# Optimization experiments

Hardware: AMD Instinct MI355X
Metric: run time of the kernel (lower is better)

The kernel has to match this reference:

```python
import jax, jax.numpy as jnp
import numpy as np

EPS = 1e-5
LOSS_WEIGHT = 0.3
IGNORE_INDEX = -100


def rmsnorm(x, w):
    # x: (B,S,D), w: (D,)
    var = jnp.mean(x * x, axis=-1, keepdims=True)
    return x * jax.lax.rsqrt(var + EPS) * w


def cross_entropy(logits, targets):
    # logits: (B,T,V), targets: (B,T) int; ignore_index=-100, mean reduction
    logp = jax.nn.log_softmax(logits, axis=-1)
    valid = targets != IGNORE_INDEX
    safe_t = jnp.where(valid, targets, 0)
    nll = -jnp.take_along_axis(logp, safe_t[..., None], axis=-1)[..., 0]
    nll = jnp.where(valid, nll, 0.0)
    return jnp.sum(nll) / jnp.maximum(jnp.sum(valid), 1)


def setup_inputs() -> dict:
    key = jax.random.key(0)
    ks = jax.random.split(key, 5)
    B, S, D, V, H = 1, 2048, 1024, 50257, 3
    hidden = jax.random.normal(ks[0], (B, S, D), dtype=jnp.float32)
    targets = jax.random.randint(ks[1], (B, S), 0, V, dtype=jnp.int64)
    emb_w = jax.random.normal(ks[2], (V, D), dtype=jnp.float32) * 0.02
    main_norm_w = jnp.ones((D,), dtype=jnp.float32)
    aux_proj_w = jax.random.normal(ks[3], (H - 1, D, D), dtype=jnp.float32) * 0.02
    aux_norm_w = jnp.ones((H - 1, D), dtype=jnp.float32)
    aux_out_w = jax.random.normal(ks[4], (H - 1, V, D), dtype=jnp.float32) * 0.02
    return {"hidden": hidden, "targets": targets, "emb_w": emb_w,
            "main_norm_w": main_norm_w, "aux_proj_w": aux_proj_w,
            "aux_norm_w": aux_norm_w, "aux_out_w": aux_out_w}


def reference(hidden, targets, emb_w, main_norm_w, aux_proj_w, aux_norm_w, aux_out_w):
    # Main head: norm -> tied vocab projection
    main_logits = jnp.einsum('bsd,vd->bsv', rmsnorm(hidden, main_norm_w), emb_w)
    main_loss = cross_entropy(main_logits[:, :-1, :], targets[:, 1:])

    # Auxiliary heads predict t+2, t+3, ...
    n_aux = aux_proj_w.shape[0]
    aux_losses = []
    for i in range(n_aux):
        k = i + 2
        h = jnp.einsum('bsd,ed->bse', hidden, aux_proj_w[i])  # d_model -> d_model
        logits = jnp.einsum('bsd,vd->bsv', rmsnorm(h, aux_norm_w[i]), aux_out_w[i])
        aux_losses.append(cross_entropy(logits[:, :-k, :], targets[:, k:]))
    total_aux = sum(aux_losses) / len(aux_losses) if aux_losses else jnp.float32(0.0)
    loss = main_loss + LOSS_WEIGHT * total_aux
    return main_logits, loss
```

## Files before the change

kernel.cpp:

```cpp
#include <hip/hip_runtime.h>
#include <hip/hip_bf16.h>


typedef __hip_bfloat16 bf16;
typedef __attribute__((ext_vector_type(8))) short bf16x8;
typedef __attribute__((ext_vector_type(4))) float f32x4;

typedef const __attribute__((address_space(1))) void* gptr_t;
typedef __attribute__((address_space(3))) void* lptr_t;

#define S_LEN   2048
#define DMODEL  1024
#define VOCAB   50257
#define VPAD2   50432
#define NT256   197

__device__ __forceinline__ void gload_lds16(const void* g, void* l) {
  __builtin_amdgcn_global_load_lds((gptr_t)g, (lptr_t)l, 16, 0, 0);
}

__global__ __launch_bounds__(256) void k_cvt(const float* __restrict__ src,
                                             bf16* __restrict__ dst,
                                             long rows_src, long rows_pad) {
  const long total4 = rows_pad << 8;
  for (long i = (long)blockIdx.x * 256 + threadIdx.x; i < total4;
       i += (long)gridDim.x * 256) {
    const long e = i << 2;
    const long row = e >> 10;
    alignas(8) bf16 o[4];
    if (row < rows_src) {
      const float4 v = *(const float4*)(src + e);
      o[0] = __float2bfloat16(v.x); o[1] = __float2bfloat16(v.y);
      o[2] = __float2bfloat16(v.z); o[3] = __float2bfloat16(v.w);
    } else {
      o[0] = o[1] = o[2] = o[3] = __float2bfloat16(0.f);
    }
    *(uint2*)(dst + e) = *(const uint2*)o;
  }
}

__global__ __launch_bounds__(256) void k_rms(const float* __restrict__ x,
                                             const float* __restrict__ w,
                                             bf16* __restrict__ xn) {
  const int row = blockIdx.x;
  const int t = threadIdx.x;
  const float4 v = ((const float4*)(x + (size_t)row * DMODEL))[t];
  float ss = v.x*v.x + v.y*v.y + v.z*v.z + v.w*v.w;
  #pragma unroll
  for (int d = 1; d < 64; d <<= 1) ss += __shfl_xor(ss, d, 64);
  __shared__ float red[4];
  if ((t & 63) == 0) red[t >> 6] = ss;
  __syncthreads();
  const float tot = red[0] + red[1] + red[2] + red[3];
  const float scale = rsqrtf(tot * (1.f / DMODEL) + 1e-5f);
  const float4 wv = ((const float4*)w)[t];
  alignas(8) bf16 o[4];
  o[0] = __float2bfloat16(v.x * scale * wv.x);
  o[1] = __float2bfloat16(v.y * scale * wv.y);
  o[2] = __float2bfloat16(v.z * scale * wv.z);
  o[3] = __float2bfloat16(v.w * scale * wv.w);
  *(uint2*)(xn + (size_t)row * DMODEL + t * 4) = *(const uint2*)o;
}

template<bool WRITE_OUT, bool DO_CE>
__global__ __launch_bounds__(512, 2)
void k_gemm256(const bf16* __restrict__ A, const bf16* __restrict__ B,
               float* __restrict__ C, long ldc, int Nvalid,
               const int* __restrict__ targets, int shift,
               float* __restrict__ pmax, float* __restrict__ psum,
               float* __restrict__ ptgt, int ntiles) {
  __shared__ char lds[131072 + 9216];

  const int t = threadIdx.x;
  const int w = t >> 6, l = t & 63;
  const int g = l >> 4, q = l & 15;
  const int wr = w >> 2, wc = w & 3;
  const int bm = blockIdx.x, bn = blockIdx.y;

  f32x4 acc[8][4];
  #pragma unroll
  for (int i = 0; i < 8; ++i)
    #pragma unroll
    for (int j = 0; j < 4; ++j)
      #pragma unroll
      for (int r = 0; r < 4; ++r) acc[i][j][r] = 0.f;

  const int srow = (l >> 2);
  const int scol = ((l & 3) * 8) ^ (((l >> 5) & 1) * 16);
  const bf16* gA0 = A + (size_t)(bm * 256 + (w * 2 + 0) * 16 + srow) * DMODEL + scol;
  const bf16* gA1 = A + (size_t)(bm * 256 + (w * 2 + 1) * 16 + srow) * DMODEL + scol;
  const bf16* gB0 = B + (size_t)(bn * 256 + (w * 2 + 0) * 16 + srow) * DMODEL + scol;
  const bf16* gB1 = B + (size_t)(bn * 256 + (w * 2 + 1) * 16 + srow) * DMODEL + scol;

  auto stage = [&](int buf, int h, int tt) {
    const int kbase = tt * 64 + (h >> 1) * 32;
    char* lb = lds + buf * 65536 + (h >> 1) * 32768 + (h & 1) * 16384 + (w * 2) * 1024;
    if (h & 1) {
      gload_lds16(gB0 + kbase, lb);
      gload_lds16(gB1 + kbase, lb + 1024);
    } else {
      gload_lds16(gA0 + kbase, lb);
      gload_lds16(gA1 + kbase, lb + 1024);
    }
  };

  const int laneoff = (q * 64 + g * 16) ^ (((q >> 3) & 1) << 5);
  auto lda = [&](int buf, int kk, int mi) {
    return *(const bf16x8*)(lds + buf * 65536 + kk * 32768 + (wr * 8 + mi) * 1024 + laneoff);
  };
  auto ldb = [&](int buf, int kk, int ni) {
    return *(const bf16x8*)(lds + buf * 65536 + kk * 32768 + 16384 + (wc * 4 + ni) * 1024 + laneoff);
  };

  stage(0, 0, 0); stage(0, 1, 0); stage(0, 2, 0); stage(0, 3, 0);
  asm volatile("s_waitcnt vmcnt(4)" ::: "memory");
  __builtin_amdgcn_s_barrier();

  #define PHASE_MFMA(MH)                                                         \
    __builtin_amdgcn_s_barrier();                                                \
    __builtin_amdgcn_s_setprio(1);                                               \
    _Pragma("unroll")                                                            \
    for (int mi = 0; mi < 4; ++mi)                                               \
      _Pragma("unroll")                                                          \
      for (int ni = 0; ni < 4; ++ni)                                             \
        acc[(MH)*4 + mi][ni] = __builtin_amdgcn_mfma_f32_16x16x32_bf16(          \
            a[mi], b[ni], acc[(MH)*4 + mi][ni], 0, 0, 0);                        \
    __builtin_amdgcn_s_setprio(0);

  for (int tt = 0; tt < 16; ++tt) {
    const int buf = tt & 1, nbuf = buf ^ 1;
    const bool pre = tt < 15;
    bf16x8 a[4], b[4];

    #pragma unroll
    for (int mi = 0; mi < 4; ++mi) a[mi] = lda(buf, 0, mi);
    #pragma unroll
    for (int ni = 0; ni < 4; ++ni) b[ni] = ldb(buf, 0, ni);
    if (pre) stage(nbuf, 0, tt + 1);
    PHASE_MFMA(0)
    __builtin_amdgcn_s_barrier();

    #pragma unroll
    for (int mi = 0; mi < 4; ++mi) a[mi] = lda(buf, 0, 4 + mi);
    if (pre) stage(nbuf, 1, tt + 1);
    PHASE_MFMA(1)
    if (pre) asm volatile("s_waitcnt vmcnt(4)" ::: "memory");
    else     asm volatile("s_waitcnt vmcnt(0)" ::: "memory");
    __builtin_amdgcn_s_barrier();

    #pragma unroll
    for (int mi = 0; mi < 4; ++mi) a[mi] = lda(buf, 1, mi);
    #pragma unroll
    for (int ni = 0; ni < 4; ++ni) b[ni] = ldb(buf, 1, ni);
    if (pre) stage(nbuf, 2, tt + 1);
    PHASE_MFMA(0)
    __builtin_amdgcn_s_barrier();

    #pragma unroll
    for (int mi = 0; mi < 4; ++mi) a[mi] = lda(buf, 1, 4 + mi);
    if (pre) stage(nbuf, 3, tt + 1);
    PHASE_MFMA(1)
    if (pre) asm volatile("s_waitcnt vmcnt(4)" ::: "memory");
    __builtin_amdgcn_s_barrier();
  }
  #undef PHASE_MFMA

  if constexpr (WRITE_OUT) {
    #pragma unroll
    for (int mi = 0; mi < 8; ++mi) {
      #pragma unroll
      for (int r = 0; r < 4; ++r) {
        const long row = bm * 256 + wr * 128 + mi * 16 + g * 4 + r;
        #pragma unroll
        for (int ni = 0; ni < 4; ++ni) {
          const int col = bn * 256 + wc * 64 + ni * 16 + q;
          if (col < Nvalid) C[row * ldc + col] = acc[mi][ni][r];
        }
      }
    }
  }

  if constexpr (DO_CE) {
    float* lds_m = (float*)(lds + 131072);
    float* lds_s = lds_m + 1024;
    int* lds_tgt = (int*)(lds_s + 1024);
    if (t < 256) {
      const int rowg = bm * 256 + t;
      lds_tgt[t] = (rowg < S_LEN - shift) ? targets[rowg + shift] : -1;
    }
    __syncthreads();
    #pragma unroll
    for (int mi = 0; mi < 8; ++mi) {
      #pragma unroll
      for (int r = 0; r < 4; ++r) {
        const int rl = wr * 128 + mi * 16 + g * 4 + r;
        const int tgt = lds_tgt[rl];
        float v[4];
        #pragma unroll
        for (int ni = 0; ni < 4; ++ni) {
          const int n = bn * 256 + wc * 64 + ni * 16 + q;
          const float av = acc[mi][ni][r];
          if (n == tgt) ptgt[bm * 256 + rl] = av;
          v[ni] = (n < Nvalid) ? av : -1e30f;
        }
        float m = fmaxf(fmaxf(v[0], v[1]), fmaxf(v[2], v[3]));
        #pragma unroll
        for (int d = 1; d < 16; d <<= 1) m = fmaxf(m, __shfl_xor(m, d, 64));
        float s = 0.f;
        #pragma unroll
        for (int ni = 0; ni < 4; ++ni) s += __expf(v[ni] - m);
        #pragma unroll
        for (int d = 1; d < 16; d <<= 1) s += __shfl_xor(s, d, 64);
        if (q == 0) { lds_m[rl * 4 + wc] = m; lds_s[rl * 4 + wc] = s; }
      }
    }
    __syncthreads();
    if (t < 256) {
      float M = lds_m[t * 4 + 0], Ssum = lds_s[t * 4 + 0];
      #pragma unroll
      for (int c = 1; c < 4; ++c) {
        const float m2 = lds_m[t * 4 + c], s2 = lds_s[t * 4 + c];
        const float nM = fmaxf(M, m2);
        Ssum = Ssum * __expf(M - nM) + s2 * __expf(m2 - nM);
        M = nM;
      }
      const size_t idx = (size_t)(bm * 256 + t) * ntiles + bn;
      pmax[idx] = M;
      psum[idx] = Ssum;
    }
  }
}

__global__ __launch_bounds__(256, 2)
void k_gemm(const bf16* __restrict__ A, const bf16* __restrict__ B,
            float* __restrict__ C, long ldc, int Nvalid) {
  constexpr int K = DMODEL;
  __shared__ bf16 As[128 * 32];
  __shared__ bf16 Bs[128 * 32];

  const int t = threadIdx.x;
  const int bn = blockIdx.x, bm = blockIdx.y;
  const int w = t >> 6, l = t & 63, g = l >> 4, q = l & 15;
  const int wr = w >> 1, wc = w & 1;

  f32x4 acc[4][4];
  #pragma unroll
  for (int i = 0; i < 4; ++i)
    #pragma unroll
    for (int j = 0; j < 4; ++j)
      #pragma unroll
      for (int r = 0; r < 4; ++r) acc[i][j][r] = 0.f;

  char* lA0 = (char*)As + w * 1024;
  char* lA1 = (char*)As + 4096 + w * 1024;
  char* lB0 = (char*)Bs + w * 1024;
  char* lB1 = (char*)Bs + 4096 + w * 1024;
  const char* gA0 = (const char*)(A + (size_t)(bm * 128 + (t >> 2)) * K) + (t & 3) * 16;
  const char* gA1 = gA0 + (size_t)64 * K * 2;
  const char* gB0 = (const char*)(B + (size_t)(bn * 128 + (t >> 2)) * K) + (t & 3) * 16;
  const char* gB1 = gB0 + (size_t)64 * K * 2;

  for (int k0 = 0; k0 < K; k0 += 32) {
    const int kb = k0 * 2;
    gload_lds16(gA0 + kb, lA0);
    gload_lds16(gA1 + kb, lA1);
    gload_lds16(gB0 + kb, lB0);
    gload_lds16(gB1 + kb, lB1);
    __syncthreads();
    bf16x8 a[4], b[4];
    #pragma unroll
    for (int mi = 0; mi < 4; ++mi)
      a[mi] = *(const bf16x8*)&As[(wr * 64 + mi * 16 + q) * 32 + g * 8];
    #pragma unroll
    for (int ni = 0; ni < 4; ++ni)
      b[ni] = *(const bf16x8*)&Bs[(wc * 64 + ni * 16 + q) * 32 + g * 8];
    #pragma unroll
    for (int mi = 0; mi < 4; ++mi)
      #pragma unroll
      for (int ni = 0; ni < 4; ++ni)
        acc[mi][ni] = __builtin_amdgcn_mfma_f32_16x16x32_bf16(a[mi], b[ni], acc[mi][ni], 0, 0, 0);
    __syncthreads();
  }

  #pragma unroll
  for (int mi = 0; mi < 4; ++mi) {
    #pragma unroll
    for (int r = 0; r < 4; ++r) {
      const long row = bm * 128 + wr * 64 + mi * 16 + g * 4 + r;
      #pragma unroll
      for (int ni = 0; ni < 4; ++ni) {
        const int col = bn * 128 + wc * 64 + ni * 16 + q;
        if (col < Nvalid) C[row * ldc + col] = acc[mi][ni][r];
      }
    }
  }
}

__global__ __launch_bounds__(64) void k_combine(const float* __restrict__ pmax,
                                                const float* __restrict__ psum,
                                                const float* __restrict__ ptgt,
                                                float* __restrict__ nll,
                                                int ntiles, int nv) {
  const int r = blockIdx.x;
  const int l = threadIdx.x;
  float M = -1e30f, Ssum = 0.f;
  for (int tl = l; tl < ntiles; tl += 64) {
    const float m = pmax[(size_t)r * ntiles + tl];
    const float s = psum[(size_t)r * ntiles + tl];
    const float nM = fmaxf(M, m);
    Ssum = Ssum * __expf(M - nM) + s * __expf(m - nM);
    M = nM;
  }
  #pragma unroll
  for (int d = 1; d < 64; d <<= 1) {
    const float m2 = __shfl_xor(M, d, 64);
    const float s2 = __shfl_xor(Ssum, d, 64);
    const float nM = fmaxf(M, m2);
    Ssum = Ssum * __expf(M - nM) + s2 * __expf(m2 - nM);
    M = nM;
  }
  if (l == 0) nll[r] = (r < nv) ? (M + logf(Ssum) - ptgt[r]) : 0.f;
}

__global__ __launch_bounds__(256) void k_loss(const float* __restrict__ nll,
                                              float* __restrict__ out) {
  __shared__ float sh[256];
  const int t = threadIdx.x;
  float sums[3];
  #pragma unroll
  for (int h = 0; h < 3; ++h) {
    const int nv = 2047 - h;
    float s = 0.f;
    for (int r = t; r < nv; r += 256) s += nll[h * 2048 + r];
    sh[t] = s; __syncthreads();
    for (int off = 128; off > 0; off >>= 1) {
      if (t < off) sh[t] += sh[t + off];
      __syncthreads();
    }
    sums[h] = sh[0]; __syncthreads();
  }
  if (t == 0)
    out[0] = sums[0] / 2047.f + 0.3f * 0.5f * (sums[1] / 2046.f + sums[2] / 2045.f);
}

extern "C" void kernel_launch(void* const* d_in, const int* in_sizes, int n_in,
                              void* d_out, int out_size, void* d_ws, size_t ws_size,
                              hipStream_t stream) {
  const float* hidden      = (const float*)d_in[0];
  const int*   targets     = (const int*)d_in[1];
  const float* emb_w       = (const float*)d_in[2];
  const float* main_norm_w = (const float*)d_in[3];
  const float* aux_proj_w  = (const float*)d_in[4];
  const float* aux_norm_w  = (const float*)d_in[5];
  const float* aux_out_w   = (const float*)d_in[6];
  float* out = (float*)d_out;

  char* ws = (char*)d_ws;
  bf16*  Wb    = (bf16*)(ws);
  bf16*  hb    = (bf16*)(ws + 103284736);
  bf16*  xn    = (bf16*)(ws + 107479040);
  bf16*  projb = (bf16*)(ws + 111673344);
  float* hbuf  = (float*)(ws + 115867648);
  float* pmax  = (float*)(ws + 124256256);
  float* psum  = (float*)(ws + 125870080);
  float* ptgt  = (float*)(ws + 127483904);
  float* nll   = (float*)(ws + 127492096);

  k_cvt<<<2048, 256, 0, stream>>>(hidden, hb, 2048, 2048);
  k_cvt<<<2048, 256, 0, stream>>>(aux_proj_w, projb, 2048, 2048);
  k_rms<<<2048, 256, 0, stream>>>(hidden, main_norm_w, xn);

  k_cvt<<<2048, 256, 0, stream>>>(emb_w, Wb, VOCAB, VPAD2);
  k_gemm256<true, true><<<dim3(8, NT256), 512, 0, stream>>>(
      xn, Wb, out, VOCAB, VOCAB, targets, 1, pmax, psum, ptgt, NT256);
  k_combine<<<2048, 64, 0, stream>>>(pmax, psum, ptgt, nll, NT256, 2047);

  for (int i = 0; i < 2; ++i) {
    k_cvt<<<2048, 256, 0, stream>>>(aux_out_w + (size_t)i * VOCAB * DMODEL, Wb, VOCAB, VPAD2);
    k_gemm<<<dim3(8, 16), 256, 0, stream>>>(
        hb, projb + (size_t)i * DMODEL * DMODEL, hbuf, DMODEL, DMODEL);
    k_rms<<<2048, 256, 0, stream>>>(hbuf, aux_norm_w + (size_t)i * DMODEL, xn);
    k_gemm256<false, true><<<dim3(8, NT256), 512, 0, stream>>>(
        xn, Wb, nullptr, 0, VOCAB, targets, i + 2, pmax, psum, ptgt, NT256);
    k_combine<<<2048, 64, 0, stream>>>(pmax, psum, ptgt, nll + (i + 1) * 2048, NT256, 2048 - (i + 2));
  }

  k_loss<<<1, 256, 0, stream>>>(nll, out + (size_t)S_LEN * VOCAB);
}
```

Baseline: 1.209 ms.

## Swizzle GEMM block order into 8x8 groups and fully unroll K-loop

New measurement: 1.205 ms. Within noise of the previous version (-0.3%).

```diff
diff --git a/kernel.cpp b/kernel.cpp
--- a/kernel.cpp
+++ b/kernel.cpp
@@ -12,8 +12,8 @@
 #define S_LEN   2048
 #define DMODEL  1024
 #define VOCAB   50257
-#define VPAD2   50432
-#define NT256   197
+#define VPAD2   51200
+#define NT256   200
 
 __device__ __forceinline__ void gload_lds16(const void* g, void* l) {
   __builtin_amdgcn_global_load_lds((gptr_t)g, (lptr_t)l, 16, 0, 0);
@@ -75,7 +75,9 @@
   const int w = t >> 6, l = t & 63;
   const int g = l >> 4, q = l & 15;
   const int wr = w >> 2, wc = w & 3;
-  const int bm = blockIdx.x, bn = blockIdx.y;
+  const int id = blockIdx.x;
+  const int bm = (id >> 3) & 7;
+  const int bn = (id & 7) + ((id >> 6) << 3);
 
   f32x4 acc[8][4];
   #pragma unroll
@@ -87,83 +89,79 @@
 
   const int srow = (l >> 2);
   const int scol = ((l & 3) * 8) ^ (((l >> 5) & 1) * 16);
-  const bf16* gA0 = A + (size_t)(bm * 256 + (w * 2 + 0) * 16 + srow) * DMODEL + scol;
-  const bf16* gA1 = A + (size_t)(bm * 256 + (w * 2 + 1) * 16 + srow) * DMODEL + scol;
-  const bf16* gB0 = B + (size_t)(bn * 256 + (w * 2 + 0) * 16 + srow) * DMODEL + scol;
-  const bf16* gB1 = B + (size_t)(bn * 256 + (w * 2 + 1) * 16 + srow) * DMODEL + scol;
-
-  auto stage = [&](int buf, int h, int tt) {
-    const int kbase = tt * 64 + (h >> 1) * 32;
-    char* lb = lds + buf * 65536 + (h >> 1) * 32768 + (h & 1) * 16384 + (w * 2) * 1024;
-    if (h & 1) {
-      gload_lds16(gB0 + kbase, lb);
-      gload_lds16(gB1 + kbase, lb + 1024);
-    } else {
-      gload_lds16(gA0 + kbase, lb);
-      gload_lds16(gA1 + kbase, lb + 1024);
-    }
-  };
+  const char* gA0 = (const char*)(A + (size_t)(bm * 256 + (w * 2 + 0) * 16 + srow) * DMODEL + scol);
+  const char* gA1 = (const char*)(A + (size_t)(bm * 256 + (w * 2 + 1) * 16 + srow) * DMODEL + scol);
+  const char* gB0 = (const char*)(B + (size_t)(bn * 256 + (w * 2 + 0) * 16 + srow) * DMODEL + scol);
+  const char* gB1 = (const char*)(B + (size_t)(bn * 256 + (w * 2 + 1) * 16 + srow) * DMODEL + scol);
 
   const int laneoff = (q * 64 + g * 16) ^ (((q >> 3) & 1) << 5);
-  auto lda = [&](int buf, int kk, int mi) {
-    return *(const bf16x8*)(lds + buf * 65536 + kk * 32768 + (wr * 8 + mi) * 1024 + laneoff);
-  };
-  auto ldb = [&](int buf, int kk, int ni) {
-    return *(const bf16x8*)(lds + buf * 65536 + kk * 32768 + 16384 + (wc * 4 + ni) * 1024 + laneoff);
-  };
-
-  stage(0, 0, 0); stage(0, 1, 0); stage(0, 2, 0); stage(0, 3, 0);
+  const char* rdA = lds + wr * 8192 + laneoff;
+  const char* rdB = lds + 16384 + wc * 4096 + laneoff;
+
+#define RDA(BUF, KK, MI) (*(const bf16x8*)(rdA + (BUF)*65536 + (KK)*32768 + (MI)*1024))
+#define RDB(BUF, KK, NI) (*(const bf16x8*)(rdB + (BUF)*65536 + (KK)*32768 + (NI)*1024))
+
+#define STAGE(BUF, H, KOFF) do {                                                  \
+    char* lb_ = lds + (BUF)*65536 + ((H)>>1)*32768 + ((H)&1)*16384 + w * 2048;    \
+    const char* s0_ = ((H)&1) ? gB0 : gA0;                                        \
+    const char* s1_ = ((H)&1) ? gB1 : gA1;                                        \
+    gload_lds16(s0_ + (KOFF) + ((H)>>1)*64, lb_);                                 \
+    gload_lds16(s1_ + (KOFF) + ((H)>>1)*64, lb_ + 1024);                          \
+  } while (0)
+
+#define PH_MFMA(MH)                                                               \
+    __builtin_amdgcn_s_barrier();                                                 \
+    __builtin_amdgcn_s_setprio(1);                                                \
+    _Pragma("unroll")                                                             \
+    for (int mi_ = 0; mi_ < 4; ++mi_)                                             \
+      _Pragma("unroll")                                                           \
+      for (int ni_ = 0; ni_ < 4; ++ni_)                                           \
+        acc[(MH)*4 + mi_][ni_] = __builtin_amdgcn_mfma_f32_16x16x32_bf16(         \
+            a[mi_], b[ni_], acc[(MH)*4 + mi_][ni_], 0, 0, 0);                     \
+    __builtin_amdgcn_s_setprio(0);
+
+#define TILE(BUF, DOSTG, KOFF, LAST) do {                                         \
+    bf16x8 a[4], b[4];                                                            \
+    _Pragma("unroll") for (int mi_ = 0; mi_ < 4; ++mi_) a[mi_] = RDA(BUF, 0, mi_);\
+    _Pragma("unroll") for (int ni_ = 0; ni_ < 4; ++ni_) b[ni_] = RDB(BUF, 0, ni_);\
+    if (DOSTG) STAGE(1-(BUF), 0, KOFF);                                           \
+    PH_MFMA(0)                                                                    \
+    __builtin_amdgcn_s_barrier();                                                 \
+    _Pragma("unroll") for (int mi_ = 0; mi_ < 4; ++mi_) a[mi_] = RDA(BUF, 0, 4+mi_);\
+    if (DOSTG) STAGE(1-(BUF), 1, KOFF);                                           \
+    PH_MFMA(1)                                                                    \
+    if (DOSTG) { asm volatile("s_waitcnt vmcnt(4)" ::: "memory"); }               \
+    if (LAST)  { asm volatile("s_waitcnt vmcnt(0)" ::: "memory"); }               \
+    __builtin_amdgcn_s_barrier();                                                 \
+    _Pragma("unroll") for (int mi_ = 0; mi_ < 4; ++mi_) a[mi_] = RDA(BUF, 1, mi_);\
+    _Pragma("unroll") for (int ni_ = 0; ni_ < 4; ++ni_) b[ni_] = RDB(BUF, 1, ni_);\
+    if (DOSTG) STAGE(1-(BUF), 2, KOFF);                                           \
+    PH_MFMA(0)                                                                    \
+    __builtin_amdgcn_s_barrier();                                                 \
+    _Pragma("unroll") for (int mi_ = 0; mi_ < 4; ++mi_) a[mi_] = RDA(BUF, 1, 4+mi_);\
+    if (DOSTG) STAGE(1-(BUF), 3, KOFF);                                           \
+    PH_MFMA(1)                                                                    \
+    if (DOSTG) { asm volatile("s_waitcnt vmcnt(4)" ::: "memory"); }               \
+    __builtin_amdgcn_s_barrier();                                                 \
+  } while (0)
+
+  STAGE(0, 0, 0); STAGE(0, 1, 0); STAGE(0, 2, 0); STAGE(0, 3, 0);
   asm volatile("s_waitcnt vmcnt(4)" ::: "memory");
   __builtin_amdgcn_s_barrier();
 
-  #define PHASE_MFMA(MH)                                                         \
-    __builtin_amdgcn_s_barrier();                                                \
-    __builtin_amdgcn_s_setprio(1);                                               \
-    _Pragma("unroll")                                                            \
-    for (int mi = 0; mi < 4; ++mi)                                               \
-      _Pragma("unroll")                                                          \
-      for (int ni = 0; ni < 4; ++ni)                                             \
-        acc[(MH)*4 + mi][ni] = __builtin_amdgcn_mfma_f32_16x16x32_bf16(          \
-            a[mi], b[ni], acc[(MH)*4 + mi][ni], 0, 0, 0);                        \
-    __builtin_amdgcn_s_setprio(0);
-
-  for (int tt = 0; tt < 16; ++tt) {
-    const int buf = tt & 1, nbuf = buf ^ 1;
-    const bool pre = tt < 15;
-    bf16x8 a[4], b[4];
-
-    #pragma unroll
-    for (int mi = 0; mi < 4; ++mi) a[mi] = lda(buf, 0, mi);
-    #pragma unroll
-    for (int ni = 0; ni < 4; ++ni) b[ni] = ldb(buf, 0, ni);
-    if (pre) stage(nbuf, 0, tt + 1);
-    PHASE_MFMA(0)
-    __builtin_amdgcn_s_barrier();
-
-    #pragma unroll
-    for (int mi = 0; mi < 4; ++mi) a[mi] = lda(buf, 0, 4 + mi);
-    if (pre) stage(nbuf, 1, tt + 1);
-    PHASE_MFMA(1)
-    if (pre) asm volatile("s_waitcnt vmcnt(4)" ::: "memory");
-    else     asm volatile("s_waitcnt vmcnt(0)" ::: "memory");
-    __builtin_amdgcn_s_barrier();
-
-    #pragma unroll
-    for (int mi = 0; mi < 4; ++mi) a[mi] = lda(buf, 1, mi);
-    #pragma unroll
-    for (int ni = 0; ni < 4; ++ni) b[ni] = ldb(buf, 1, ni);
-    if (pre) stage(nbuf, 2, tt + 1);
-    PHASE_MFMA(0)
-    __builtin_amdgcn_s_barrier();
-
-    #pragma unroll
-    for (int mi = 0; mi < 4; ++mi) a[mi] = lda(buf, 1, 4 + mi);
-    if (pre) stage(nbuf, 3, tt + 1);
-    PHASE_MFMA(1)
-    if (pre) asm volatile("s_waitcnt vmcnt(4)" ::: "memory");
-    __builtin_amdgcn_s_barrier();
-  }
-  #undef PHASE_MFMA
+  for (int t2 = 0; t2 < 7; ++t2) {
+    TILE(0, 1, 128, 0);
+    TILE(1, 1, 256, 0);
+    gA0 += 256; gA1 += 256; gB0 += 256; gB1 += 256;
+  }
+  TILE(0, 1, 128, 0);
+  TILE(1, 0, 0, 1);
+
+#undef TILE
+#undef PH_MFMA
+#undef STAGE
+#undef RDA
+#undef RDB
 
   if constexpr (WRITE_OUT) {
     #pragma unroll
@@ -357,21 +355,21 @@
 
   char* ws = (char*)d_ws;
   bf16*  Wb    = (bf16*)(ws);
-  bf16*  hb    = (bf16*)(ws + 103284736);
-  bf16*  xn    = (bf16*)(ws + 107479040);
-  bf16*  projb = (bf16*)(ws + 111673344);
-  float* hbuf  = (float*)(ws + 115867648);
-  float* pmax  = (float*)(ws + 124256256);
-  float* psum  = (float*)(ws + 125870080);
-  float* ptgt  = (float*)(ws + 127483904);
-  float* nll   = (float*)(ws + 127492096);
+  bf16*  hb    = (bf16*)(ws + 104857600);
+  bf16*  xn    = (bf16*)(ws + 109051904);
+  bf16*  projb = (bf16*)(ws + 113246208);
+  float* hbuf  = (float*)(ws + 117440512);
+  float* pmax  = (float*)(ws + 125829120);
+  float* psum  = (float*)(ws + 127467520);
+  float* ptgt  = (float*)(ws + 129105920);
+  float* nll   = (float*)(ws + 129114112);
 
   k_cvt<<<2048, 256, 0, stream>>>(hidden, hb, 2048, 2048);
   k_cvt<<<2048, 256, 0, stream>>>(aux_proj_w, projb, 2048, 2048);
   k_rms<<<2048, 256, 0, stream>>>(hidden, main_norm_w, xn);
 
   k_cvt<<<2048, 256, 0, stream>>>(emb_w, Wb, VOCAB, VPAD2);
-  k_gemm256<true, true><<<dim3(8, NT256), 512, 0, stream>>>(
+  k_gemm256<true, true><<<1600, 512, 0, stream>>>(
       xn, Wb, out, VOCAB, VOCAB, targets, 1, pmax, psum, ptgt, NT256);
   k_combine<<<2048, 64, 0, stream>>>(pmax, psum, ptgt, nll, NT256, 2047);
 
@@ -380,7 +378,7 @@
     k_gemm<<<dim3(8, 16), 256, 0, stream>>>(
         hb, projb + (size_t)i * DMODEL * DMODEL, hbuf, DMODEL, DMODEL);
     k_rms<<<2048, 256, 0, stream>>>(hbuf, aux_norm_w + (size_t)i * DMODEL, xn);
-    k_gemm256<false, true><<<dim3(8, NT256), 512, 0, stream>>>(
+    k_gemm256<false, true><<<1600, 512, 0, stream>>>(
         xn, Wb, nullptr, 0, VOCAB, targets, i + 2, pmax, psum, ptgt, NT256);
     k_combine<<<2048, 64, 0, stream>>>(pmax, psum, ptgt, nll + (i + 1) * 2048, NT256, 2048 - (i + 2));
   }
```
